# Performance work log

Measured on AMD Instinct MI355X. Metric: run time of the kernel, lower is better.

The kernel has to match this reference:

```python
import jax, jax.numpy as jnp
import numpy as np

# ---- static config (matches init_kwargs) ----
B, N, D, FH, FW, C = 2, 6, 48, 16, 44, 80
OGH, OGW, DOWNSAMPLE = 256, 704, 16
D_MIN, D_MAX = 2.0, 58.0
XB = (-51.2, 51.2, 0.4); YB = (-51.2, 51.2, 0.4); ZB = (-10.0, 10.0, 20.0)
NX, NY, NZ = 256, 256, 1  # (ub-lb)/step per bound
DX = jnp.array([XB[2], YB[2], ZB[2]], jnp.float32)
LOWER = jnp.array([XB[0], YB[0], ZB[0]], jnp.float32)  # bx - dx/2


def _frustum():
    # UD depth discretization: d_i = d_min + i*(d_max-d_min)/D
    ds = D_MIN + (D_MAX - D_MIN) / D * np.arange(D, dtype=np.float32)
    ds = np.broadcast_to(ds[:, None, None], (D, FH, FW))
    xs = np.broadcast_to(np.linspace(0, OGW - 1, FW, dtype=np.float32)[None, None, :], (D, FH, FW))
    ys = np.broadcast_to(np.linspace(0, OGH - 1, FH, dtype=np.float32)[None, :, None], (D, FH, FW))
    return jnp.asarray(np.stack([xs, ys, ds], -1))  # [D,FH,FW,3]

FRUSTUM = _frustum()


def setup_inputs() -> dict:
    key = jax.random.key(0)
    k1, k2 = jax.random.split(key)
    x = jax.random.normal(k1, (B, N, D, FH, FW, C), dtype=jnp.float32)
    # camera-to-ego rotation: ego_x = z_cam (fwd), ego_y = -x_cam, ego_z = -y_cam
    R = np.array([[0.0, 0.0, 1.0], [-1.0, 0.0, 0.0], [0.0, -1.0, 0.0]], np.float32)
    rots = jnp.asarray(np.broadcast_to(R, (B, N, 3, 3)).copy())
    trans = 2.0 * jax.random.normal(k2, (B, N, 3), dtype=jnp.float32)
    K = np.array([[500.0, 0.0, OGW / 2.0], [0.0, 500.0, OGH / 2.0], [0.0, 0.0, 1.0]], np.float32)
    intrins = jnp.asarray(np.broadcast_to(K, (B, N, 3, 3)).copy())
    post_rots = jnp.asarray(np.broadcast_to(np.eye(3, dtype=np.float32), (B, N, 3, 3)).copy())
    post_trans = jnp.zeros((B, N, 3), jnp.float32)
    return {"x": x, "rots": rots, "trans": trans, "intrins": intrins,
            "post_rots": post_rots, "post_trans": post_trans}


def _get_geometry(rots, trans, intrins, post_rots, post_trans):
    # frustum -> ego-frame 3D points: [B,N,D,FH,FW,3]
    pts = FRUSTUM[None, None] - post_trans[:, :, None, None, None, :]
    inv_post = jnp.linalg.inv(post_rots)
    pts = jnp.einsum('bnij,bndhwj->bndhwi', inv_post, pts)
    # un-normalize pixel coords by depth
    pts = jnp.concatenate([pts[..., :2] * pts[..., 2:3], pts[..., 2:3]], axis=-1)
    combine = jnp.einsum('bnij,bnjk->bnik', rots, jnp.linalg.inv(intrins))
    pts = jnp.einsum('bnij,bndhwj->bndhwi', combine, pts)
    return pts + trans[:, :, None, None, None, :]


def _voxel_pooling(geom, x):
    Nprime = B * N * D * FH * FW
    xf = x.reshape(Nprime, C)
    # voxel indices; torch .long() truncates toward zero -> astype matches
    gi = ((geom.reshape(Nprime, 3) - LOWER) / DX).astype(jnp.int32)
    batch_ix = jnp.repeat(jnp.arange(B, dtype=jnp.int32), Nprime // B)
    kept = ((gi[:, 0] >= 0) & (gi[:, 0] < NX) &
            (gi[:, 1] >= 0) & (gi[:, 1] < NY) &
            (gi[:, 2] >= 0) & (gi[:, 2] < NZ))
    gi = jnp.where(kept[:, None], gi, 0)
    # flat index into (B, NZ, NY, NX); equivalent aggregation to sort+quickcumsum
    flat = ((batch_ix * NZ + gi[:, 2]) * NY + gi[:, 1]) * NX + gi[:, 0]
    xm = jnp.where(kept[:, None], xf, 0.0)
    pooled = jax.ops.segment_sum(xm, flat, num_segments=B * NZ * NY * NX)
    final = pooled.reshape(B, NZ, NY, NX, C).transpose(0, 4, 1, 2, 3)
    return final  # [B, C, NZ, NY, NX]


def reference(x, rots, trans, intrins, post_rots, post_trans):
    geom = _get_geometry(rots, trans, intrins, post_rots, post_trans)
    return _voxel_pooling(geom, x)
```

## Files before the change

### kernel.cpp

```cpp
#include <hip/hip_runtime.h>
#include <hip/hip_bf16.h>


#define NCH       80
#define GRID_HW   65536
#define OUT_PER_B 5242880
#define HSTRIDE   3520
#define PTS_PER_BN 33792
#define S_FLOATS  10485760
#define S_BYTES   41943040

__device__ inline void inv3(const double a[9], double inv[9]) {
    double c00 =  a[4]*a[8] - a[5]*a[7];
    double c01 = -(a[3]*a[8] - a[5]*a[6]);
    double c02 =  a[3]*a[7] - a[4]*a[6];
    double det = a[0]*c00 + a[1]*c01 + a[2]*c02;
    double id  = 1.0/det;
    inv[0] = c00*id;
    inv[1] = (a[2]*a[7]-a[1]*a[8])*id;
    inv[2] = (a[1]*a[5]-a[2]*a[4])*id;
    inv[3] = c01*id;
    inv[4] = (a[0]*a[8]-a[2]*a[6])*id;
    inv[5] = (a[2]*a[3]-a[0]*a[5])*id;
    inv[6] = c02*id;
    inv[7] = (a[1]*a[6]-a[0]*a[7])*id;
    inv[8] = (a[0]*a[4]-a[1]*a[3])*id;
}

__global__ void prep_kernel(const float* __restrict__ rots,
                            const float* __restrict__ trans,
                            const float* __restrict__ intrins,
                            const float* __restrict__ post_rots,
                            const float* __restrict__ post_trans,
                            double* __restrict__ tw) {
    int bn = threadIdx.x;
    if (bn >= 12) return;
    double pr[9], kk[9], rt[9], ipr[9], ik[9];
    #pragma unroll
    for (int i = 0; i < 9; i++) {
        pr[i] = (double)post_rots[bn*9 + i];
        kk[i] = (double)intrins[bn*9 + i];
        rt[i] = (double)rots[bn*9 + i];
    }
    inv3(pr, ipr);
    inv3(kk, ik);
    double* o = tw + bn*24;
    #pragma unroll
    for (int i = 0; i < 9; i++) o[i] = ipr[i];
    #pragma unroll
    for (int r = 0; r < 3; r++)
        #pragma unroll
        for (int c = 0; c < 3; c++)
            o[9 + r*3 + c] = rt[r*3+0]*ik[0*3+c] + rt[r*3+1]*ik[1*3+c] + rt[r*3+2]*ik[2*3+c];
    #pragma unroll
    for (int i = 0; i < 3; i++) o[18 + i] = (double)post_trans[bn*3 + i];
    #pragma unroll
    for (int i = 0; i < 3; i++) o[21 + i] = (double)trans[bn*3 + i];
}

__global__ __launch_bounds__(256) void zero_kernel(float4* __restrict__ p, int n4) {
    int i = blockIdx.x * 256 + threadIdx.x;
    int stride = gridDim.x * 256;
    for (; i < n4; i += stride) p[i] = make_float4(0.f, 0.f, 0.f, 0.f);
}

__device__ inline void geom_phase(const double* __restrict__ ws,
                                  int bn, int d, int tid,
                                  int* s_base, int* s_colbase,
                                  unsigned* s_mask, unsigned* s_fb) {
    const int b = bn / 6;
    const double* t = ws + bn * 24;
    const float dsv = __fadd_rn(2.0f, __fmul_rn((float)(56.0 / 48.0), (float)d));

    for (int idx = tid; idx < 704; idx += 256) {
        const int h = idx / 44;
        const int w = idx - h * 44;
        float xsv = (w == 43) ? 703.0f : (float)((double)w * (703.0 / 43.0));
        float ysv = (float)(h * 17);

        double px = (double)xsv - t[18];
        double py = (double)ysv - t[19];
        double pz = (double)dsv - t[20];
        double q0 = t[0]*px + t[1]*py + t[2]*pz;
        double q1 = t[3]*px + t[4]*py + t[5]*pz;
        double q2 = t[6]*px + t[7]*py + t[8]*pz;
        q0 *= q2;
        q1 *= q2;
        double e0 = t[9]*q0  + t[10]*q1 + t[11]*q2 + t[21];
        double e1 = t[12]*q0 + t[13]*q1 + t[14]*q2 + t[22];
        double e2 = t[15]*q0 + t[16]*q1 + t[17]*q2 + t[23];

        const double lxy = (double)(-51.2f);
        const double dxy = (double)(0.4f);
        int gx = (int)((e0 - lxy) / dxy);
        int gy = (int)((e1 - lxy) / dxy);
        int gz = (int)((e2 - (double)(-10.0f)) / (double)(20.0f));
        int base = -1;
        if (gx >= 0 && gx < 256 && gy >= 0 && gy < 256 && gz == 0)
            base = (b << 16) | (gy << 8) | gx;
        s_base[idx] = base;
    }
    __syncthreads();

    if (tid < 44) {
        int cb = -1; unsigned mm = 0, fb = 0;
        #pragma unroll
        for (int h = 0; h < 16; h++) {
            int pb = s_base[h * 44 + tid];
            if (pb >= 0) {
                if (cb < 0) cb = pb;
                if (pb == cb) mm |= (1u << h);
                else          fb |= (1u << h);
            }
        }
        s_colbase[tid] = cb;
        s_mask[tid]    = mm;
        s_fb[tid]      = fb;
    }
    __syncthreads();
}

__global__ __launch_bounds__(256) void scatter_grid_kernel(const float* __restrict__ x,
                                                           const double* __restrict__ ws,
                                                           float* __restrict__ S) {
    __shared__ int      s_base[704];
    __shared__ int      s_colbase[44];
    __shared__ unsigned s_mask[44];
    __shared__ unsigned s_fb[44];

    const int tid = threadIdx.x;
    const int bn  = blockIdx.x / 48;
    const int d   = blockIdx.x - bn * 48;
    geom_phase(ws, bn, d, tid, s_base, s_colbase, s_mask, s_fb);

    const float* xb0 = x + ((size_t)bn * PTS_PER_BN + (size_t)d * 704) * NCH;
    #pragma unroll
    for (int pass = 0; pass < 4; pass++) {
        int item = pass * 256 + tid;
        if (item >= 880) break;
        int w  = item / 20;
        int c4 = item - w * 20;
        unsigned mm = s_mask[w];
        unsigned fb = s_fb[w];
        if (!(mm | fb)) continue;
        const float* xb = xb0 + (size_t)w * NCH + c4 * 4;
        float ax = 0.f, ay = 0.f, az = 0.f, aw = 0.f;
        #pragma unroll
        for (int h = 0; h < 16; h++) {
            if ((mm >> h) & 1u) {
                float4 v = *(const float4*)(xb + h * HSTRIDE);
                ax += v.x; ay += v.y; az += v.z; aw += v.w;
            } else if ((fb >> h) & 1u) {
                float4 v = *(const float4*)(xb + h * HSTRIDE);
                float* sp = S + (size_t)s_base[h * 44 + w] * NCH + c4 * 4;
                atomicAdd(sp + 0, v.x);
                atomicAdd(sp + 1, v.y);
                atomicAdd(sp + 2, v.z);
                atomicAdd(sp + 3, v.w);
            }
        }
        if (mm) {
            float* sp = S + (size_t)s_colbase[w] * NCH + c4 * 4;
            atomicAdd(sp + 0, ax);
            atomicAdd(sp + 1, ay);
            atomicAdd(sp + 2, az);
            atomicAdd(sp + 3, aw);
        }
    }
}

__global__ __launch_bounds__(256) void transpose_kernel(const float* __restrict__ S,
                                                        float* __restrict__ out) {
    __shared__ float tile[64 * 81];
    const int tid = threadIdx.x;
    const int b   = blockIdx.x >> 10;
    const int v0  = (blockIdx.x & 1023) * 64;
    const float* src = S + ((size_t)(b << 16) + v0) * NCH;
    #pragma unroll
    for (int i = 0; i < 20; i++) {
        int j = i * 256 + tid;
        int v = j / 80;
        int c = j - v * 80;
        tile[v * 81 + c] = src[j];
    }
    __syncthreads();
    float* dst = out + (size_t)b * OUT_PER_B + v0;
    #pragma unroll
    for (int i = 0; i < 20; i++) {
        int k  = i * 256 + tid;
        int c  = k >> 6;
        int lv = k & 63;
        dst[(size_t)c * GRID_HW + lv] = tile[lv * 81 + c];
    }
}

__global__ __launch_bounds__(256) void scatter_direct_kernel(const float* __restrict__ x,
                                                             const double* __restrict__ ws,
                                                             float* __restrict__ out) {
    __shared__ int      s_base[704];
    __shared__ int      s_colbase[44];
    __shared__ unsigned s_mask[44];
    __shared__ unsigned s_fb[44];

    const int tid = threadIdx.x;
    const int bn  = blockIdx.x / 48;
    const int d   = blockIdx.x - bn * 48;
    geom_phase(ws, bn, d, tid, s_base, s_colbase, s_mask, s_fb);

    const float* xb0 = x + ((size_t)bn * PTS_PER_BN + (size_t)d * 704) * NCH;
    #pragma unroll
    for (int pass = 0; pass < 4; pass++) {
        int item = pass * 256 + tid;
        if (item >= 880) break;
        int w  = item / 20;
        int c4 = item - w * 20;
        unsigned mm = s_mask[w];
        unsigned fb = s_fb[w];
        if (!(mm | fb)) continue;
        const float* xb = xb0 + (size_t)w * NCH + c4 * 4;
        float ax = 0.f, ay = 0.f, az = 0.f, aw = 0.f;
        #pragma unroll
        for (int h = 0; h < 16; h++) {
            if ((mm >> h) & 1u) {
                float4 v = *(const float4*)(xb + h * HSTRIDE);
                ax += v.x; ay += v.y; az += v.z; aw += v.w;
            } else if ((fb >> h) & 1u) {
                float4 v = *(const float4*)(xb + h * HSTRIDE);
                int vb = s_base[h * 44 + w];
                float* o = out + (size_t)(vb >> 16) * OUT_PER_B + (vb & 65535);
                atomicAdd(o + (size_t)(c4*4 + 0) * GRID_HW, v.x);
                atomicAdd(o + (size_t)(c4*4 + 1) * GRID_HW, v.y);
                atomicAdd(o + (size_t)(c4*4 + 2) * GRID_HW, v.z);
                atomicAdd(o + (size_t)(c4*4 + 3) * GRID_HW, v.w);
            }
        }
        if (mm) {
            int vb = s_colbase[w];
            float* o = out + (size_t)(vb >> 16) * OUT_PER_B + (vb & 65535);
            atomicAdd(o + (size_t)(c4*4 + 0) * GRID_HW, ax);
            atomicAdd(o + (size_t)(c4*4 + 1) * GRID_HW, ay);
            atomicAdd(o + (size_t)(c4*4 + 2) * GRID_HW, az);
            atomicAdd(o + (size_t)(c4*4 + 3) * GRID_HW, aw);
        }
    }
}

extern "C" void kernel_launch(void* const* d_in, const int* in_sizes, int n_in,
                              void* d_out, int out_size, void* d_ws, size_t ws_size,
                              hipStream_t stream) {
    const float* x          = (const float*)d_in[0];
    const float* rots       = (const float*)d_in[1];
    const float* trans      = (const float*)d_in[2];
    const float* intrins    = (const float*)d_in[3];
    const float* post_rots  = (const float*)d_in[4];
    const float* post_trans = (const float*)d_in[5];
    float* out = (float*)d_out;

    if (ws_size >= (size_t)S_BYTES + 4096) {
        float*  S  = (float*)d_ws;
        double* tw = (double*)((char*)d_ws + S_BYTES);
        zero_kernel<<<2560, 256, 0, stream>>>((float4*)S, S_FLOATS / 4);
        prep_kernel<<<1, 64, 0, stream>>>(rots, trans, intrins, post_rots, post_trans, tw);
        scatter_grid_kernel<<<576, 256, 0, stream>>>(x, tw, S);
        transpose_kernel<<<2048, 256, 0, stream>>>(S, out);
    } else {
        double* tw = (double*)d_ws;
        zero_kernel<<<2560, 256, 0, stream>>>((float4*)out, out_size / 4);
        prep_kernel<<<1, 64, 0, stream>>>(rots, trans, intrins, post_rots, post_trans, tw);
        scatter_direct_kernel<<<576, 256, 0, stream>>>(x, tw, out);
    }
}
```

Baseline: 239.2 us.

## Replace atomic dense-grid scatter with compacted partials and per-voxel linked lists

Instead of zeroing a dense voxel-major grid and accumulating with float atomics, each block sums column runs per distinct voxel into a compact partial buffer and links entries into per-voxel lists via atomicExch on a head array. A gather kernel walks the lists per voxel and writes the channel-major output through a shared-memory transpose. This removes the grid zeroing pass and most floating-point atomic traffic, at the cost of a larger workspace requirement and pointer-chasing reads in the gather. Camera matrix prep is also folded into the scatter kernel.

Measured after the change: 250.5 us. +4.7%, slower.

```diff
diff --git a/kernel.cpp b/kernel.cpp
--- a/kernel.cpp
+++ b/kernel.cpp
@@ -1,5 +1,4 @@
 #include <hip/hip_runtime.h>
-#include <hip/hip_bf16.h>
 
 
 #define NCH       80
@@ -7,8 +6,13 @@
 #define OUT_PER_B 5242880
 #define HSTRIDE   3520
 #define PTS_PER_BN 33792
-#define S_FLOATS  10485760
-#define S_BYTES   41943040
+
+#define N_ENT_MAX 405504
+#define P_BYTES   129761280u
+#define NEXT_OFF  129761280u
+#define HEAD_OFF  131383296u
+#define CNT_OFF   131907584u
+#define WS_NEED   131907588u
 
 __device__ inline void inv3(const double a[9], double inv[9]) {
     double c00 =  a[4]*a[8] - a[5]*a[7];
@@ -27,6 +31,34 @@
     inv[8] = (a[0]*a[4]-a[1]*a[3])*id;
 }
 
+__device__ inline void prep_bn(const float* __restrict__ rots,
+                               const float* __restrict__ trans,
+                               const float* __restrict__ intrins,
+                               const float* __restrict__ post_rots,
+                               const float* __restrict__ post_trans,
+                               int bn, double* o) {
+    double pr[9], kk[9], rt[9], ipr[9], ik[9];
+    #pragma unroll
+    for (int i = 0; i < 9; i++) {
+        pr[i] = (double)post_rots[bn*9 + i];
+        kk[i] = (double)intrins[bn*9 + i];
+        rt[i] = (double)rots[bn*9 + i];
+    }
+    inv3(pr, ipr);
+    inv3(kk, ik);
+    #pragma unroll
+    for (int i = 0; i < 9; i++) o[i] = ipr[i];
+    #pragma unroll
+    for (int r = 0; r < 3; r++)
+        #pragma unroll
+        for (int c = 0; c < 3; c++)
+            o[9 + r*3 + c] = rt[r*3+0]*ik[0*3+c] + rt[r*3+1]*ik[1*3+c] + rt[r*3+2]*ik[2*3+c];
+    #pragma unroll
+    for (int i = 0; i < 3; i++) o[18 + i] = (double)post_trans[bn*3 + i];
+    #pragma unroll
+    for (int i = 0; i < 3; i++) o[21 + i] = (double)trans[bn*3 + i];
+}
+
 __global__ void prep_kernel(const float* __restrict__ rots,
                             const float* __restrict__ trans,
                             const float* __restrict__ intrins,
@@ -35,27 +67,7 @@
                             double* __restrict__ tw) {
     int bn = threadIdx.x;
     if (bn >= 12) return;
-    double pr[9], kk[9], rt[9], ipr[9], ik[9];
-    #pragma unroll
-    for (int i = 0; i < 9; i++) {
-        pr[i] = (double)post_rots[bn*9 + i];
-        kk[i] = (double)intrins[bn*9 + i];
-        rt[i] = (double)rots[bn*9 + i];
-    }
-    inv3(pr, ipr);
-    inv3(kk, ik);
-    double* o = tw + bn*24;
-    #pragma unroll
-    for (int i = 0; i < 9; i++) o[i] = ipr[i];
-    #pragma unroll
-    for (int r = 0; r < 3; r++)
-        #pragma unroll
-        for (int c = 0; c < 3; c++)
-            o[9 + r*3 + c] = rt[r*3+0]*ik[0*3+c] + rt[r*3+1]*ik[1*3+c] + rt[r*3+2]*ik[2*3+c];
-    #pragma unroll
-    for (int i = 0; i < 3; i++) o[18 + i] = (double)post_trans[bn*3 + i];
-    #pragma unroll
-    for (int i = 0; i < 3; i++) o[21 + i] = (double)trans[bn*3 + i];
+    prep_bn(rots, trans, intrins, post_rots, post_trans, bn, tw + bn*24);
 }
 
 __global__ __launch_bounds__(256) void zero_kernel(float4* __restrict__ p, int n4) {
@@ -64,14 +76,15 @@
     for (; i < n4; i += stride) p[i] = make_float4(0.f, 0.f, 0.f, 0.f);
 }
 
-__device__ inline void geom_phase(const double* __restrict__ ws,
-                                  int bn, int d, int tid,
-                                  int* s_base, int* s_colbase,
-                                  unsigned* s_mask, unsigned* s_fb) {
-    const int b = bn / 6;
-    const double* t = ws + bn * 24;
+__global__ __launch_bounds__(256) void init_heads(int* __restrict__ head, int* __restrict__ counter) {
+    int i = blockIdx.x * 256 + threadIdx.x;
+    if (i < 131072) head[i] = -1;
+    if (i == 0) counter[0] = 0;
+}
+
+__device__ inline void geom_points(const double* __restrict__ t,
+                                   int b, int d, int tid, int* s_base) {
     const float dsv = __fadd_rn(2.0f, __fmul_rn((float)(56.0 / 48.0), (float)d));
-
     for (int idx = tid; idx < 704; idx += 256) {
         const int h = idx / 44;
         const int w = idx - h * 44;
@@ -100,6 +113,150 @@
             base = (b << 16) | (gy << 8) | gx;
         s_base[idx] = base;
     }
+}
+
+__global__ __launch_bounds__(256) void scatter_compact(const float* __restrict__ x,
+                                                       const float* __restrict__ rots,
+                                                       const float* __restrict__ trans,
+                                                       const float* __restrict__ intrins,
+                                                       const float* __restrict__ post_rots,
+                                                       const float* __restrict__ post_trans,
+                                                       float* __restrict__ P,
+                                                       int* __restrict__ nxt,
+                                                       int* __restrict__ head,
+                                                       int* __restrict__ counter) {
+    __shared__ double   s_t[24];
+    __shared__ int      s_base[704];
+    __shared__ int      s_gbase[704];
+    __shared__ unsigned s_gmask[704];
+    __shared__ int      s_gcount[44];
+    __shared__ int      s_goff[44];
+    __shared__ short    s_gslot[704];
+    __shared__ int      s_eb, s_G;
+
+    const int tid = threadIdx.x;
+    const int bn  = blockIdx.x / 48;
+    const int d   = blockIdx.x - bn * 48;
+    const int b   = bn / 6;
+
+    if (tid == 0)
+        prep_bn(rots, trans, intrins, post_rots, post_trans, bn, s_t);
+    __syncthreads();
+
+    geom_points(s_t, b, d, tid, s_base);
+    __syncthreads();
+
+    if (tid < 44) {
+        int gb[16]; unsigned gm[16];
+        int cnt = 0;
+        #pragma unroll
+        for (int h = 0; h < 16; h++) {
+            int pb = s_base[h * 44 + tid];
+            if (pb >= 0) {
+                int j = 0;
+                for (; j < cnt; j++) if (gb[j] == pb) break;
+                if (j < cnt) gm[j] |= (1u << h);
+                else { gb[cnt] = pb; gm[cnt] = (1u << h); cnt++; }
+            }
+        }
+        s_gcount[tid] = cnt;
+        for (int j = 0; j < cnt; j++) {
+            s_gbase[tid * 16 + j] = gb[j];
+            s_gmask[tid * 16 + j] = gm[j];
+        }
+    }
+    __syncthreads();
+
+    if (tid == 0) {
+        int off = 0;
+        for (int w = 0; w < 44; w++) { s_goff[w] = off; off += s_gcount[w]; }
+        s_G  = off;
+        s_eb = atomicAdd(counter, off);
+    }
+    __syncthreads();
+
+    if (tid < 44) {
+        int off = s_goff[tid];
+        int cnt = s_gcount[tid];
+        for (int k = 0; k < cnt; k++) {
+            int g = off + k;
+            s_gslot[g] = (short)((tid << 4) | k);
+            int e = s_eb + g;
+            nxt[e] = atomicExch(&head[s_gbase[tid * 16 + k]], e);
+        }
+    }
+    __syncthreads();
+
+    const int G  = s_G;
+    const int eb = s_eb;
+    const float* xb0 = x + ((size_t)bn * PTS_PER_BN + (size_t)d * 704) * NCH;
+    for (int item = tid; item < G * 20; item += 256) {
+        int g  = item / 20;
+        int c4 = item - g * 20;
+        int slot = (int)s_gslot[g];
+        int w = slot >> 4;
+        int k = slot & 15;
+        unsigned mm = s_gmask[w * 16 + k];
+        const float* xb = xb0 + (size_t)w * NCH + c4 * 4;
+        float ax = 0.f, ay = 0.f, az = 0.f, aw = 0.f;
+        #pragma unroll
+        for (int h = 0; h < 16; h++) {
+            if ((mm >> h) & 1u) {
+                float4 v = *(const float4*)(xb + h * HSTRIDE);
+                ax += v.x; ay += v.y; az += v.z; aw += v.w;
+            }
+        }
+        float4 r; r.x = ax; r.y = ay; r.z = az; r.w = aw;
+        *(float4*)(P + (size_t)(eb + g) * NCH + c4 * 4) = r;
+    }
+}
+
+__global__ __launch_bounds__(256) void gather_kernel(const float* __restrict__ P,
+                                                     const int* __restrict__ nxt,
+                                                     const int* __restrict__ head,
+                                                     float* __restrict__ out) {
+    __shared__ float tile[64 * 81];
+    const int tid = threadIdx.x;
+    const int b   = blockIdx.x >> 10;
+    const int v0  = (blockIdx.x & 1023) * 64;
+    const int* hb = head + (b << 16) + v0;
+    #pragma unroll
+    for (int i = 0; i < 20; i++) {
+        int j = i * 256 + tid;
+        int v = j / 80;
+        int c = j - v * 80;
+        float s = 0.f;
+        int e = hb[v];
+        while (e >= 0) {
+            s += P[(size_t)e * NCH + c];
+            e = nxt[e];
+        }
+        tile[v * 81 + c] = s;
+    }
+    __syncthreads();
+    float* dst = out + (size_t)b * OUT_PER_B + v0;
+    #pragma unroll
+    for (int i = 0; i < 20; i++) {
+        int k  = i * 256 + tid;
+        int c  = k >> 6;
+        int lv = k & 63;
+        dst[(size_t)c * GRID_HW + lv] = tile[lv * 81 + c];
+    }
+}
+
+__global__ __launch_bounds__(256) void scatter_direct_kernel(const float* __restrict__ x,
+                                                             const double* __restrict__ ws,
+                                                             float* __restrict__ out) {
+    __shared__ int      s_base[704];
+    __shared__ int      s_colbase[44];
+    __shared__ unsigned s_mask[44];
+    __shared__ unsigned s_fb[44];
+
+    const int tid = threadIdx.x;
+    const int bn  = blockIdx.x / 48;
+    const int d   = blockIdx.x - bn * 48;
+    const int b   = bn / 6;
+    geom_points(ws + bn * 24, b, d, tid, s_base);
     __syncthreads();
 
     if (tid < 44) {
@@ -118,94 +275,6 @@
         s_fb[tid]      = fb;
     }
     __syncthreads();
-}
-
-__global__ __launch_bounds__(256) void scatter_grid_kernel(const float* __restrict__ x,
-                                                           const double* __restrict__ ws,
-                                                           float* __restrict__ S) {
-    __shared__ int      s_base[704];
-    __shared__ int      s_colbase[44];
-    __shared__ unsigned s_mask[44];
-    __shared__ unsigned s_fb[44];
-
-    const int tid = threadIdx.x;
-    const int bn  = blockIdx.x / 48;
-    const int d   = blockIdx.x - bn * 48;
-    geom_phase(ws, bn, d, tid, s_base, s_colbase, s_mask, s_fb);
-
-    const float* xb0 = x + ((size_t)bn * PTS_PER_BN + (size_t)d * 704) * NCH;
-    #pragma unroll
-    for (int pass = 0; pass < 4; pass++) {
-        int item = pass * 256 + tid;
-        if (item >= 880) break;
-        int w  = item / 20;
-        int c4 = item - w * 20;
-        unsigned mm = s_mask[w];
-        unsigned fb = s_fb[w];
-        if (!(mm | fb)) continue;
-        const float* xb = xb0 + (size_t)w * NCH + c4 * 4;
-        float ax = 0.f, ay = 0.f, az = 0.f, aw = 0.f;
-        #pragma unroll
-        for (int h = 0; h < 16; h++) {
-            if ((mm >> h) & 1u) {
-                float4 v = *(const float4*)(xb + h * HSTRIDE);
-                ax += v.x; ay += v.y; az += v.z; aw += v.w;
-            } else if ((fb >> h) & 1u) {
-                float4 v = *(const float4*)(xb + h * HSTRIDE);
-                float* sp = S + (size_t)s_base[h * 44 + w] * NCH + c4 * 4;
-                atomicAdd(sp + 0, v.x);
-                atomicAdd(sp + 1, v.y);
-                atomicAdd(sp + 2, v.z);
-                atomicAdd(sp + 3, v.w);
-            }
-        }
-        if (mm) {
-            float* sp = S + (size_t)s_colbase[w] * NCH + c4 * 4;
-            atomicAdd(sp + 0, ax);
-            atomicAdd(sp + 1, ay);
-            atomicAdd(sp + 2, az);
-            atomicAdd(sp + 3, aw);
-        }
-    }
-}
-
-__global__ __launch_bounds__(256) void transpose_kernel(const float* __restrict__ S,
-                                                        float* __restrict__ out) {
-    __shared__ float tile[64 * 81];
-    const int tid = threadIdx.x;
-    const int b   = blockIdx.x >> 10;
-    const int v0  = (blockIdx.x & 1023) * 64;
-    const float* src = S + ((size_t)(b << 16) + v0) * NCH;
-    #pragma unroll
-    for (int i = 0; i < 20; i++) {
-        int j = i * 256 + tid;
-        int v = j / 80;
-        int c = j - v * 80;
-        tile[v * 81 + c] = src[j];
-    }
-    __syncthreads();
-    float* dst = out + (size_t)b * OUT_PER_B + v0;
-    #pragma unroll
-    for (int i = 0; i < 20; i++) {
-        int k  = i * 256 + tid;
-        int c  = k >> 6;
-        int lv = k & 63;
-        dst[(size_t)c * GRID_HW + lv] = tile[lv * 81 + c];
-    }
-}
-
-__global__ __launch_bounds__(256) void scatter_direct_kernel(const float* __restrict__ x,
-                                                             const double* __restrict__ ws,
-                                                             float* __restrict__ out) {
-    __shared__ int      s_base[704];
-    __shared__ int      s_colbase[44];
-    __shared__ unsigned s_mask[44];
-    __shared__ unsigned s_fb[44];
-
-    const int tid = threadIdx.x;
-    const int bn  = blockIdx.x / 48;
-    const int d   = blockIdx.x - bn * 48;
-    geom_phase(ws, bn, d, tid, s_base, s_colbase, s_mask, s_fb);
 
     const float* xb0 = x + ((size_t)bn * PTS_PER_BN + (size_t)d * 704) * NCH;
     #pragma unroll
@@ -256,16 +325,19 @@
     const float* post_trans = (const float*)d_in[5];
     float* out = (float*)d_out;
 
-    if (ws_size >= (size_t)S_BYTES + 4096) {
-        float*  S  = (float*)d_ws;
-        double* tw = (double*)((char*)d_ws + S_BYTES);
-        zero_kernel<<<2560, 256, 0, stream>>>((float4*)S, S_FLOATS / 4);
-        prep_kernel<<<1, 64, 0, stream>>>(rots, trans, intrins, post_rots, post_trans, tw);
-        scatter_grid_kernel<<<576, 256, 0, stream>>>(x, tw, S);
-        transpose_kernel<<<2048, 256, 0, stream>>>(S, out);
-    } else {
+    if (ws_size >= (size_t)WS_NEED) {
+        float* P       = (float*)d_ws;
+        int*   nxt     = (int*)((char*)d_ws + NEXT_OFF);
+        int*   head    = (int*)((char*)d_ws + HEAD_OFF);
+        int*   counter = (int*)((char*)d_ws + CNT_OFF);
+        init_heads<<<512, 256, 0, stream>>>(head, counter);
+        scatter_compact<<<576, 256, 0, stream>>>(x, rots, trans, intrins,
+                                                 post_rots, post_trans,
+                                                 P, nxt, head, counter);
+        gather_kernel<<<2048, 256, 0, stream>>>(P, nxt, head, out);
+    } else if (ws_size >= 12 * 24 * sizeof(double)) {
         double* tw = (double*)d_ws;
-        zero_kernel<<<2560, 256, 0, stream>>>((float4*)out, out_size / 4);
+        zero_kernel<<<2560, 256, 0, stream>>>((float4*)out, out_size / 16);
         prep_kernel<<<1, 64, 0, stream>>>(rots, trans, intrins, post_rots, post_trans, tw);
         scatter_direct_kernel<<<576, 256, 0, stream>>>(x, tw, out);
     }
```
